# Optimization experiments

Hardware: AMD Instinct MI355X
Metric: run time of the kernel (lower is better)

## Reference

```python
import jax, jax.numpy as jnp
import numpy as np

B = 64  # batch_size (number of graphs)


def _leaky(v):
    return jax.nn.leaky_relu(v, 0.01)


def _gine(x, src, dst, edge_attr, ew, eb, w1, b1, w2, b2):
    # GINEConv (eps=0): out = nn(x + sum_{j->i} relu(x_j + lin(edge_attr)))
    n = x.shape[0]
    msg = jax.nn.relu(x[src] + edge_attr @ ew + eb)      # [E, C]
    agg = jax.ops.segment_sum(msg, dst, num_segments=n)  # [N, C]
    h = x + agg
    h = _leaky(h @ w1 + b1)
    h = _leaky(h @ w2 + b2)
    return h


def setup_inputs() -> dict:
    key = jax.random.key(0)
    ks = jax.random.split(key, 32)
    N, E, NF, EF, H, A = 65536, 1048576, 32, 16, 128, 10
    s = 0.05
    inp = {
        'x': jax.random.normal(ks[0], (N, NF), jnp.float32),
        'edge_index': jax.random.randint(ks[1], (2, E), 0, N, jnp.int64)
        if jax.config.jax_enable_x64 else jax.random.randint(ks[1], (2, E), 0, N, jnp.int32),
        'edge_attr': jax.random.normal(ks[2], (E, EF), jnp.float32),
        'e1_w': jax.random.normal(ks[3], (EF, NF)) * s, 'e1_b': jnp.zeros((NF,)),
        'c1_w1': jax.random.normal(ks[4], (NF, H)) * s, 'c1_b1': jnp.zeros((H,)),
        'c1_w2': jax.random.normal(ks[5], (H, H)) * s, 'c1_b2': jnp.zeros((H,)),
        'e2_w': jax.random.normal(ks[6], (EF, H)) * s, 'e2_b': jnp.zeros((H,)),
        'c2_w1': jax.random.normal(ks[7], (H, H)) * s, 'c2_b1': jnp.zeros((H,)),
        'c2_w2': jax.random.normal(ks[8], (H, H)) * s, 'c2_b2': jnp.zeros((H,)),
        'a_w1': jax.random.normal(ks[9], (H, H)) * s, 'a_b1': jnp.zeros((H,)),
        'a_w2': jax.random.normal(ks[10], (H, A)) * s, 'a_b2': jnp.zeros((A,)),
        'n_w1': jax.random.normal(ks[11], (H, H)) * s, 'n_b1': jnp.zeros((H,)),
        'n_w2': jax.random.normal(ks[12], (H, H)) * s, 'n_b2': jnp.zeros((H,)),
        'n_w3': jax.random.normal(ks[13], (H, 1)) * s, 'n_b3': jnp.zeros((1,)),
    }
    return inp


def reference(x, edge_index, edge_attr,
              e1_w, e1_b, c1_w1, c1_b1, c1_w2, c1_b2,
              e2_w, e2_b, c2_w1, c2_b1, c2_w2, c2_b2,
              a_w1, a_b1, a_w2, a_b2,
              n_w1, n_b1, n_w2, n_b2, n_w3, n_b3):
    src, dst = edge_index[0], edge_index[1]
    h = _gine(x, src, dst, edge_attr, e1_w, e1_b, c1_w1, c1_b1, c1_w2, c1_b2)
    h = jax.nn.relu(h)  # dropout is identity in eval mode
    h = _gine(h, src, dst, edge_attr, e2_w, e2_b, c2_w1, c2_b1, c2_w2, c2_b2)
    H = h.shape[-1]
    hb = h.reshape(B, -1, H)            # [B, Nper, H]
    pooled = hb.mean(axis=1)            # [B, H]
    a = _leaky(_leaky(pooled @ a_w1 + a_b1) @ a_w2 + a_b2)
    action_prob = jax.nn.softmax(a, axis=1)
    # reinterpret flat node order as [Nper, B, H], as in the torch reshape
    xr = h.reshape(-1, B, H)
    nh = _leaky(xr @ n_w1 + n_b1)
    nh = _leaky(nh @ n_w2 + n_b2)
    node_scores = jax.nn.sigmoid(nh @ n_w3 + n_b3)[..., 0].T  # [B, Nper]
    return action_prob, node_scores
```

## Files before the change

### kernel.cpp

```cpp
#include <hip/hip_runtime.h>
#include <math.h>

#define NNODES 65536
#define NEDGES 1048576
#define NF 32
#define EF 16
#define HD 128
#define NACT 10
#define NB 64
#define NPER 1024

typedef unsigned short u16;
typedef float  vf2  __attribute__((ext_vector_type(2)));
typedef float  vf4  __attribute__((ext_vector_type(4)));
typedef __bf16 vbf8 __attribute__((ext_vector_type(8)));
#define BC8(v) __builtin_bit_cast(vbf8, v)
#define WB() __builtin_amdgcn_wave_barrier()

__device__ __forceinline__ float leakyf(float v) { return v > 0.0f ? v : 0.01f * v; }
__device__ __forceinline__ vf2 fma2(vf2 a, vf2 b, vf2 c) { return __builtin_elementwise_fma(a, b, c); }
__device__ __forceinline__ vf2 max2(vf2 a, vf2 b) { return __builtin_elementwise_max(a, b); }
__device__ __forceinline__ vf2 splat2(float s) { vf2 r = {s, s}; return r; }

__device__ __forceinline__ u16 f2bf(float x) {
    unsigned u = __float_as_uint(x);
    return (u16)((u + 0x7FFFu + ((u >> 16) & 1u)) >> 16);
}
__device__ __forceinline__ float bf2f(u16 h) { return __uint_as_float(((unsigned)h) << 16); }

__device__ __forceinline__ void cvt4(const float4 s, uint2& hi, uint2& lo) {
    const u16 h0 = f2bf(s.x), h1 = f2bf(s.y), h2 = f2bf(s.z), h3 = f2bf(s.w);
    hi = make_uint2((unsigned)h0 | ((unsigned)h1 << 16), (unsigned)h2 | ((unsigned)h3 << 16));
    const u16 l0 = f2bf(s.x - bf2f(h0)), l1 = f2bf(s.y - bf2f(h1));
    const u16 l2 = f2bf(s.z - bf2f(h2)), l3 = f2bf(s.w - bf2f(h3));
    lo = make_uint2((unsigned)l0 | ((unsigned)l1 << 16), (unsigned)l2 | ((unsigned)l3 << 16));
}
__device__ __forceinline__ uint2 cvt4hi(const float4 s) {
    const u16 h0 = f2bf(s.x), h1 = f2bf(s.y), h2 = f2bf(s.z), h3 = f2bf(s.w);
    return make_uint2((unsigned)h0 | ((unsigned)h1 << 16), (unsigned)h2 | ((unsigned)h3 << 16));
}

__global__ __launch_bounds__(256) void hist_kernel(const int* __restrict__ ei, int* __restrict__ cnt)
{
    const int i = blockIdx.x * 256 + threadIdx.x;
    if (i < NEDGES) atomicAdd(&cnt[ei[NEDGES + i]], 1);
}

__global__ __launch_bounds__(1024) void scan_kernel(const int* __restrict__ cnt, int* __restrict__ rs)
{
    __shared__ int s[1024];
    const int t = threadIdx.x;
    int loc[64];
    int tot = 0;
    const int4* c4 = (const int4*)(cnt + t * 64);
    #pragma unroll
    for (int j = 0; j < 16; ++j) {
        const int4 v = c4[j];
        loc[4*j+0] = v.x; loc[4*j+1] = v.y; loc[4*j+2] = v.z; loc[4*j+3] = v.w;
        tot += v.x + v.y + v.z + v.w;
    }
    s[t] = tot;
    __syncthreads();
    for (int off = 1; off < 1024; off <<= 1) {
        const int v = (t >= off) ? s[t - off] : 0;
        __syncthreads();
        s[t] += v;
        __syncthreads();
    }
    int run = s[t] - tot;
    #pragma unroll
    for (int j = 0; j < 64; ++j) { rs[t * 64 + j] = run; run += loc[j]; }
    if (t == 0) rs[NNODES] = NEDGES;
}

__global__ __launch_bounds__(256) void scatter_kernel(
    const int* __restrict__ ei, const int* __restrict__ rs, int* __restrict__ fill,
    int* __restrict__ ssrc, int* __restrict__ seidx)
{
    const int i = blockIdx.x * 256 + threadIdx.x;
    if (i < NEDGES) {
        const int d = ei[NEDGES + i];
        const int pos = rs[d] + atomicAdd(&fill[d], 1);
        ssrc[pos]  = ei[i];
        seidx[pos] = i;
    }
}

__global__ __launch_bounds__(256) void permute_kernel(
    const int* __restrict__ seidx, const float* __restrict__ ea, float* __restrict__ sea)
{
    const int t = blockIdx.x * 256 + threadIdx.x;
    const int e = t >> 2, part = t & 3;
    const int idx = seidx[e];
    ((float4*)sea)[(size_t)e * 4 + part] = ((const float4*)ea)[(size_t)idx * 4 + part];
}

__global__ __launch_bounds__(256) void pack_all_kernel(
    const float* __restrict__ w0, const float* __restrict__ w1, const float* __restrict__ w2,
    const float* __restrict__ w3, const float* __restrict__ w4, const float* __restrict__ w5,
    u16* __restrict__ pw)
{
    const int bid = blockIdx.x;
    const float* W; int KB, seg, sbase;
    if (bid < 16) { W = w0; KB = 1; seg = 0; sbase = 0; }
    else {
        const int i = (bid - 16) >> 6;
        seg = i + 1; sbase = 16 + i * 64; KB = 4;
        W = (i == 0) ? w1 : (i == 1) ? w2 : (i == 2) ? w3 : (i == 3) ? w4 : w5;
    }
    const int t = (bid - sbase) * 256 + threadIdx.x;
    const int j = t & 7, lane = (t >> 3) & 63, rest = t >> 9;
    const int kb = rest % KB, fb = rest / KB;
    if (fb >= 8) return;
    const int k = kb * 32 + (lane >> 4) * 8 + j;
    const int f = fb * 16 + (lane & 15);
    const float val = W[k * HD + f];
    const u16 h = f2bf(val);
    u16* dst = pw + seg * 32768;
    dst[t] = h;
    dst[16384 + t] = f2bf(val - bf2f(h));
}

__global__ __launch_bounds__(256) void e1_agg_kernel(
    const float* __restrict__ x, const int* __restrict__ rs,
    const int* __restrict__ ssrc, const float* __restrict__ sea,
    const float* __restrict__ w, const float* __restrict__ b, float* __restrict__ agg)
{
    const int tid  = threadIdx.x;
    const int lane = tid & 63;
    const int p    = lane & 15;
    const int q    = lane >> 4;
    const int node = blockIdx.x * 4 + (tid >> 6);
    vf2 wr[EF];
    #pragma unroll
    for (int k = 0; k < EF; ++k) wr[k] = *(const vf2*)&w[k * NF + p * 2];
    const vf2 bias = *(const vf2*)&b[p * 2];
    const int beg = rs[node], end = rs[node + 1];
    vf2 acc = {0.0f, 0.0f};
    for (int e = beg + q; e < end; e += 4) {
        const int sA = ssrc[e];
        const float4* pA = (const float4*)sea + (size_t)e * 4;
        const float4 A0 = pA[0], A1 = pA[1], A2 = pA[2], A3 = pA[3];
        const vf2 xv = *(const vf2*)((const char*)x + (((unsigned)sA << 7) + (unsigned)p * 8));
        vf2 m = bias;
        m = fma2(splat2(A0.x), wr[0],  m); m = fma2(splat2(A0.y), wr[1],  m);
        m = fma2(splat2(A0.z), wr[2],  m); m = fma2(splat2(A0.w), wr[3],  m);
        m = fma2(splat2(A1.x), wr[4],  m); m = fma2(splat2(A1.y), wr[5],  m);
        m = fma2(splat2(A1.z), wr[6],  m); m = fma2(splat2(A1.w), wr[7],  m);
        m = fma2(splat2(A2.x), wr[8],  m); m = fma2(splat2(A2.y), wr[9],  m);
        m = fma2(splat2(A2.z), wr[10], m); m = fma2(splat2(A2.w), wr[11], m);
        m = fma2(splat2(A3.x), wr[12], m); m = fma2(splat2(A3.y), wr[13], m);
        m = fma2(splat2(A3.z), wr[14], m); m = fma2(splat2(A3.w), wr[15], m);
        acc += max2(xv + m, splat2(0.0f));
    }
    acc[0] += __shfl_xor(acc[0], 16, 64); acc[1] += __shfl_xor(acc[1], 16, 64);
    acc[0] += __shfl_xor(acc[0], 32, 64); acc[1] += __shfl_xor(acc[1], 32, 64);
    if (lane < 16) *(vf2*)&agg[(size_t)node * NF + p * 2] = acc;
}

__global__ __launch_bounds__(256) void e2_agg_kernel(
    const float* __restrict__ h, const int* __restrict__ rs,
    const int* __restrict__ ssrc, const float* __restrict__ sea,
    const float* __restrict__ w, const float* __restrict__ b, float* __restrict__ agg)
{
    const int tid  = threadIdx.x;
    const int lane = tid & 63;
    const unsigned foff = (unsigned)lane * 8;
    const int node = blockIdx.x * 4 + (tid >> 6);
    vf2 wr[EF];
    #pragma unroll
    for (int k = 0; k < EF; ++k) wr[k] = *(const vf2*)&w[k * HD + lane * 2];
    const vf2 bias = *(const vf2*)&b[lane * 2];
    const int beg = __builtin_amdgcn_readfirstlane(rs[node]);
    const int end = __builtin_amdgcn_readfirstlane(rs[node + 1]);
    vf2 acc = {0.0f, 0.0f};
    int e = beg;
    for (; e + 2 <= end; e += 2) {
        const int sA = ssrc[e];
        const int sB = ssrc[e + 1];
        const vf2 hA = *(const vf2*)((const char*)h + (((unsigned)sA << 9) + foff));
        const vf2 hB = *(const vf2*)((const char*)h + (((unsigned)sB << 9) + foff));
        const float* aA = &sea[(size_t)e * EF];
        const float* aB = aA + EF;
        vf2 mA = bias, mB = bias;
        #pragma unroll
        for (int k = 0; k < EF; ++k) {
            mA = fma2(splat2(aA[k]), wr[k], mA);
            mB = fma2(splat2(aB[k]), wr[k], mB);
        }
        acc += max2(hA + mA, splat2(0.0f));
        acc += max2(hB + mB, splat2(0.0f));
    }
    if (e < end) {
        const int sA = ssrc[e];
        const vf2 hA = *(const vf2*)((const char*)h + (((unsigned)sA << 9) + foff));
        const float* aA = &sea[(size_t)e * EF];
        vf2 mA = bias;
        #pragma unroll
        for (int k = 0; k < EF; ++k) mA = fma2(splat2(aA[k]), wr[k], mA);
        acc += max2(hA + mA, splat2(0.0f));
    }
    *(vf2*)&agg[(size_t)node * HD + lane * 2] = acc;
}

#define ROW128 272
#define ROW32  80

__device__ __forceinline__ void mfma_layer128_in(
    const unsigned char* __restrict__ aH, const unsigned char* __restrict__ aL,
    const u16* __restrict__ wH, const u16* __restrict__ wL,
    const float* __restrict__ bias, int lane, vf4* __restrict__ acc)
{
    const int quad = lane >> 4, fm = lane & 15;
    int4 Bh[4], Bl[4];
    #pragma unroll
    for (int kb = 0; kb < 4; ++kb) {
        Bh[kb] = *(const int4*)(aH + fm * ROW128 + kb * 64 + quad * 16);
        Bl[kb] = *(const int4*)(aL + fm * ROW128 + kb * 64 + quad * 16);
    }
    #pragma unroll
    for (int fb = 0; fb < 8; ++fb) {
        const float4 bv = *(const float4*)&bias[fb * 16 + quad * 4];
        vf4 a = {bv.x, bv.y, bv.z, bv.w};
        #pragma unroll
        for (int kb = 0; kb < 4; ++kb) {
            const int4 wh = *(const int4*)(wH + ((fb * 4 + kb) * 64 + lane) * 8);
            const int4 wl = *(const int4*)(wL + ((fb * 4 + kb) * 64 + lane) * 8);
            a = __builtin_amdgcn_mfma_f32_16x16x32_bf16(BC8(wh), BC8(Bl[kb]), a, 0, 0, 0);
            a = __builtin_amdgcn_mfma_f32_16x16x32_bf16(BC8(wl), BC8(Bh[kb]), a, 0, 0, 0);
            a = __builtin_amdgcn_mfma_f32_16x16x32_bf16(BC8(wh), BC8(Bh[kb]), a, 0, 0, 0);
        }
        acc[fb] = a;
    }
}

__device__ __forceinline__ void mfma_layer128_act(
    const unsigned char* __restrict__ aH,
    const u16* __restrict__ wH, const u16* __restrict__ wL,
    const float* __restrict__ bias, int lane, vf4* __restrict__ acc)
{
    const int quad = lane >> 4, fm = lane & 15;
    int4 Bh[4];
    #pragma unroll
    for (int kb = 0; kb < 4; ++kb)
        Bh[kb] = *(const int4*)(aH + fm * ROW128 + kb * 64 + quad * 16);
    #pragma unroll
    for (int fb = 0; fb < 8; ++fb) {
        const float4 bv = *(const float4*)&bias[fb * 16 + quad * 4];
        vf4 a = {bv.x, bv.y, bv.z, bv.w};
        #pragma unroll
        for (int kb = 0; kb < 4; ++kb) {
            const int4 wh = *(const int4*)(wH + ((fb * 4 + kb) * 64 + lane) * 8);
            const int4 wl = *(const int4*)(wL + ((fb * 4 + kb) * 64 + lane) * 8);
            a = __builtin_amdgcn_mfma_f32_16x16x32_bf16(BC8(wl), BC8(Bh[kb]), a, 0, 0, 0);
            a = __builtin_amdgcn_mfma_f32_16x16x32_bf16(BC8(wh), BC8(Bh[kb]), a, 0, 0, 0);
        }
        acc[fb] = a;
    }
}

__device__ __forceinline__ void mfma_layer32_in(
    const unsigned char* __restrict__ aH, const unsigned char* __restrict__ aL,
    const u16* __restrict__ wH, const u16* __restrict__ wL,
    const float* __restrict__ bias, int lane, vf4* __restrict__ acc)
{
    const int quad = lane >> 4, fm = lane & 15;
    const int4 Bh = *(const int4*)(aH + fm * ROW32 + quad * 16);
    const int4 Bl = *(const int4*)(aL + fm * ROW32 + quad * 16);
    #pragma unroll
    for (int fb = 0; fb < 8; ++fb) {
        const float4 bv = *(const float4*)&bias[fb * 16 + quad * 4];
        vf4 a = {bv.x, bv.y, bv.z, bv.w};
        const int4 wh = *(const int4*)(wH + (fb * 64 + lane) * 8);
        const int4 wl = *(const int4*)(wL + (fb * 64 + lane) * 8);
        a = __builtin_amdgcn_mfma_f32_16x16x32_bf16(BC8(wh), BC8(Bl), a, 0, 0, 0);
        a = __builtin_amdgcn_mfma_f32_16x16x32_bf16(BC8(wl), BC8(Bh), a, 0, 0, 0);
        a = __builtin_amdgcn_mfma_f32_16x16x32_bf16(BC8(wh), BC8(Bh), a, 0, 0, 0);
        acc[fb] = a;
    }
}

__device__ __forceinline__ void store_act_hi(
    unsigned char* __restrict__ aH, int lane, vf4* __restrict__ acc)
{
    const int quad = lane >> 4, fm = lane & 15;
    #pragma unroll
    for (int fb = 0; fb < 8; ++fb) {
        const float4 s = {leakyf(acc[fb][0]), leakyf(acc[fb][1]), leakyf(acc[fb][2]), leakyf(acc[fb][3])};
        acc[fb][0] = s.x; acc[fb][1] = s.y; acc[fb][2] = s.z; acc[fb][3] = s.w;
        *(uint2*)(aH + fm * ROW128 + fb * 32 + quad * 8) = cvt4hi(s);
    }
}

__global__ __launch_bounds__(256) void n1_kernel(
    const float* __restrict__ x, const float* __restrict__ agg,
    const u16* __restrict__ w1h, const u16* __restrict__ w1l, const float* __restrict__ b1,
    const u16* __restrict__ w2h, const u16* __restrict__ w2l, const float* __restrict__ b2,
    float* __restrict__ hout)
{
    __shared__ __align__(16) unsigned char smem[4][2560 + 16 * ROW128];
    const int tid = threadIdx.x, lane = tid & 63, wid = tid >> 6;
    const int quad = lane >> 4, fm = lane & 15;
    const int tile = blockIdx.x * 4 + wid;
    unsigned char* inH = smem[wid];
    unsigned char* inL = inH + 16 * ROW32;
    unsigned char* aH  = inH + 2560;
    const size_t base = (size_t)tile * 16 * NF;
    #pragma unroll
    for (int i = 0; i < 2; ++i) {
        const int flat = i * 64 + lane;
        const int node = flat >> 3, kq = flat & 7;
        const float4 xv = *(const float4*)&x[base + node * NF + kq * 4];
        const float4 av = *(const float4*)&agg[base + node * NF + kq * 4];
        const float4 s = {xv.x + av.x, xv.y + av.y, xv.z + av.z, xv.w + av.w};
        uint2 phi, plo;
        cvt4(s, phi, plo);
        *(uint2*)(inH + node * ROW32 + kq * 8) = phi;
        *(uint2*)(inL + node * ROW32 + kq * 8) = plo;
    }
    WB();
    vf4 acc[8];
    mfma_layer32_in(inH, inL, w1h, w1l, b1, lane, acc);
    WB();
    store_act_hi(aH, lane, acc);
    WB();
    mfma_layer128_act(aH, w2h, w2l, b2, lane, acc);
    const size_t ob = (size_t)tile * 16 * HD;
    #pragma unroll
    for (int fb = 0; fb < 8; ++fb) {
        const float4 o = {fmaxf(acc[fb][0], 0.0f), fmaxf(acc[fb][1], 0.0f),
                          fmaxf(acc[fb][2], 0.0f), fmaxf(acc[fb][3], 0.0f)};
        *(float4*)&hout[ob + fm * HD + fb * 16 + quad * 4] = o;
    }
}

__global__ __launch_bounds__(256) void n2_kernel(
    const float* __restrict__ h, const float* __restrict__ agg,
    const u16* __restrict__ w1h, const u16* __restrict__ w1l, const float* __restrict__ b1,
    const u16* __restrict__ w2h, const u16* __restrict__ w2l, const float* __restrict__ b2,
    const u16* __restrict__ m1h, const u16* __restrict__ m1l, const float* __restrict__ nb1,
    const u16* __restrict__ m2h, const u16* __restrict__ m2l, const float* __restrict__ nb2,
    const float* __restrict__ nw3, const float* __restrict__ nb3,
    float* __restrict__ pooled, float* __restrict__ scores)
{
    __shared__ __align__(16) unsigned char smem[4][2 * 16 * ROW128];
    const int tid = threadIdx.x, lane = tid & 63, wid = tid >> 6;
    const int quad = lane >> 4, fm = lane & 15;
    const int tile = blockIdx.x * 4 + wid;
    unsigned char* aH = smem[wid];
    unsigned char* aL = aH + 16 * ROW128;
    const size_t base = (size_t)tile * 16 * HD;
    #pragma unroll
    for (int i = 0; i < 8; ++i) {
        const int flat = i * 64 + lane;
        const int node = flat >> 5, kq = flat & 31;
        const float4 hv = *(const float4*)&h[base + node * HD + kq * 4];
        const float4 av = *(const float4*)&agg[base + node * HD + kq * 4];
        const float4 s = {hv.x + av.x, hv.y + av.y, hv.z + av.z, hv.w + av.w};
        uint2 phi, plo;
        cvt4(s, phi, plo);
        *(uint2*)(aH + node * ROW128 + kq * 8) = phi;
        *(uint2*)(aL + node * ROW128 + kq * 8) = plo;
    }
    WB();
    vf4 acc[8];
    mfma_layer128_in(aH, aL, w1h, w1l, b1, lane, acc);
    WB();
    store_act_hi(aH, lane, acc);
    WB();
    mfma_layer128_act(aH, w2h, w2l, b2, lane, acc);
    WB();
    store_act_hi(aH, lane, acc);
    {
        const int g = tile >> 6;
        #pragma unroll
        for (int fb = 0; fb < 8; ++fb) {
            vf4 t = acc[fb];
            #pragma unroll
            for (int off = 1; off < 16; off <<= 1) {
                t[0] += __shfl_xor(t[0], off, 64);
                t[1] += __shfl_xor(t[1], off, 64);
                t[2] += __shfl_xor(t[2], off, 64);
                t[3] += __shfl_xor(t[3], off, 64);
            }
            #pragma unroll
            for (int r = 0; r < 4; ++r) {
                const int item = fb * 4 + r;
                if (fm == (item >> 1))
                    atomicAdd(&pooled[g * HD + fb * 16 + quad * 4 + r], t[r]);
            }
        }
    }
    WB();
    mfma_layer128_act(aH, m1h, m1l, nb1, lane, acc);
    WB();
    store_act_hi(aH, lane, acc);
    WB();
    mfma_layer128_act(aH, m2h, m2l, nb2, lane, acc);
    float v = 0.0f;
    #pragma unroll
    for (int fb = 0; fb < 8; ++fb) {
        const float4 w3v = *(const float4*)&nw3[fb * 16 + quad * 4];
        v += leakyf(acc[fb][0]) * w3v.x + leakyf(acc[fb][1]) * w3v.y
           + leakyf(acc[fb][2]) * w3v.z + leakyf(acc[fb][3]) * w3v.w;
    }
    v += __shfl_xor(v, 16, 64);
    v += __shfl_xor(v, 32, 64);
    if (lane < 16) {
        const int node = tile * 16 + fm;
        const float s = v + nb3[0];
        scores[(node & 63) * NPER + (node >> 6)] = 1.0f / (1.0f + expf(-s));
    }
}

__global__ __launch_bounds__(128) void act_kernel(
    const float* __restrict__ pooled,
    const float* __restrict__ w1, const float* __restrict__ b1,
    const float* __restrict__ w2, const float* __restrict__ b2,
    float* __restrict__ out)
{
    __shared__ __align__(16) float p[HD];
    __shared__ float a1[HD];
    __shared__ float z[NACT];
    __shared__ float red2[2];
    const int g = blockIdx.x;
    const int tid = threadIdx.x;
    p[tid] = pooled[g * HD + tid] * (1.0f / NPER);
    __syncthreads();
    float acc = b1[tid];
    for (int k = 0; k < HD; ++k) acc = fmaf(p[k], w1[k * HD + tid], acc);
    a1[tid] = leakyf(acc);
    __syncthreads();
    if (tid < NACT) {
        float a2 = b2[tid];
        for (int k = 0; k < HD; ++k) a2 = fmaf(a1[k], w2[k * NACT + tid], a2);
        z[tid] = leakyf(a2);
    }
    __syncthreads();
    if (tid == 0) {
        float m = z[0];
        for (int i = 1; i < NACT; ++i) m = fmaxf(m, z[i]);
        red2[0] = m;
    }
    __syncthreads();
    if (tid < NACT) z[tid] = expf(z[tid] - red2[0]);
    __syncthreads();
    if (tid == 0) {
        float s = 0.0f;
        for (int i = 0; i < NACT; ++i) s += z[i];
        red2[1] = s;
    }
    __syncthreads();
    if (tid < NACT) out[g * NACT + tid] = z[tid] / red2[1];
}

extern "C" void kernel_launch(void* const* d_in, const int* in_sizes, int n_in,
                              void* d_out, int out_size, void* d_ws, size_t ws_size,
                              hipStream_t stream)
{
    const float* x    = (const float*)d_in[0];
    const int*   ei   = (const int*)d_in[1];
    const float* ea   = (const float*)d_in[2];
    const float* e1w  = (const float*)d_in[3];
    const float* e1b  = (const float*)d_in[4];
    const float* c1w1 = (const float*)d_in[5];
    const float* c1b1 = (const float*)d_in[6];
    const float* c1w2 = (const float*)d_in[7];
    const float* c1b2 = (const float*)d_in[8];
    const float* e2w  = (const float*)d_in[9];
    const float* e2b  = (const float*)d_in[10];
    const float* c2w1 = (const float*)d_in[11];
    const float* c2b1 = (const float*)d_in[12];
    const float* c2w2 = (const float*)d_in[13];
    const float* c2b2 = (const float*)d_in[14];
    const float* aw1  = (const float*)d_in[15];
    const float* ab1  = (const float*)d_in[16];
    const float* aw2  = (const float*)d_in[17];
    const float* ab2  = (const float*)d_in[18];
    const float* nw1  = (const float*)d_in[19];
    const float* nb1  = (const float*)d_in[20];
    const float* nw2  = (const float*)d_in[21];
    const float* nb2  = (const float*)d_in[22];
    const float* nw3  = (const float*)d_in[23];
    const float* nb3  = (const float*)d_in[24];

    float* out = (float*)d_out;
    char*  ws  = (char*)d_ws;
    const size_t MB = 1024 * 1024;
    float* h      = (float*)(ws);
    float* agg2   = (float*)(ws + 32  * MB);
    int*   seidx  = (int*)  (ws + 32  * MB);
    float* sea    = (float*)(ws + 64  * MB);
    float* agg1   = (float*)(ws + 128 * MB);
    float* pooled = (float*)(ws + 136 * MB);
    u16*   pw     = (u16*)  (ws + 136 * MB + 64 * 1024);
    int*   cnt    = (int*)  (ws + 137 * MB);
    int*   fill   = (int*)  (ws + 137 * MB + 256 * 1024);
    int*   rs     = (int*)  (ws + 139 * MB);
    int*   ssrc   = (int*)  (ws + 140 * MB);

    u16* p_c1w1 = pw;
    u16* p_c1w2 = pw + 1 * 32768;
    u16* p_c2w1 = pw + 2 * 32768;
    u16* p_c2w2 = pw + 3 * 32768;
    u16* p_nw1  = pw + 4 * 32768;
    u16* p_nw2  = pw + 5 * 32768;

    hipMemsetAsync(cnt,    0, 2 * NNODES * sizeof(int), stream);
    hipMemsetAsync(pooled, 0, (size_t)NB * HD * sizeof(float), stream);

    pack_all_kernel<<<336, 256, 0, stream>>>(c1w1, c1w2, c2w1, c2w2, nw1, nw2, pw);

    hist_kernel<<<NEDGES / 256, 256, 0, stream>>>(ei, cnt);
    scan_kernel<<<1, 1024, 0, stream>>>(cnt, rs);
    scatter_kernel<<<NEDGES / 256, 256, 0, stream>>>(ei, rs, fill, ssrc, seidx);
    permute_kernel<<<NEDGES / 64, 256, 0, stream>>>(seidx, ea, sea);

    e1_agg_kernel<<<NNODES / 4, 256, 0, stream>>>(x, rs, ssrc, sea, e1w, e1b, agg1);
    n1_kernel<<<NNODES / 64, 256, 0, stream>>>(x, agg1,
                                               p_c1w1, p_c1w1 + 16384, c1b1,
                                               p_c1w2, p_c1w2 + 16384, c1b2, h);
    e2_agg_kernel<<<NNODES / 4, 256, 0, stream>>>(h, rs, ssrc, sea, e2w, e2b, agg2);
    n2_kernel<<<NNODES / 64, 256, 0, stream>>>(h, agg2,
                                               p_c2w1, p_c2w1 + 16384, c2b1,
                                               p_c2w2, p_c2w2 + 16384, c2b2,
                                               p_nw1,  p_nw1  + 16384, nb1,
                                               p_nw2,  p_nw2  + 16384, nb2,
                                               nw3, nb3, pooled, out + NB * NACT);
    act_kernel<<<NB, 128, 0, stream>>>(pooled, aw1, ab1, aw2, ab2, out);
}
```

Measured before the change: 576.9 us.

## Coalesce edge-attr loads in e1 aggregation and broadcast via ds_swizzle

Rewrites the e1 aggregation loop so that each wave loads edge attributes as coalesced scalar floats, one per lane, instead of four redundant float4 loads per lane. Each attribute is then broadcast within its 16-lane group using ds_swizzle for the FMA chain. Source indices are loaded once per 64-edge window and distributed with shuffles, and the row bounds are made wave-uniform with readfirstlane. This aims to cut redundant global memory traffic, at the cost of extra cross-lane operations and more complex tail handling.

```diff
diff --git a/kernel.cpp b/kernel.cpp
--- a/kernel.cpp
+++ b/kernel.cpp
@@ -38,6 +38,14 @@
 __device__ __forceinline__ uint2 cvt4hi(const float4 s) {
     const u16 h0 = f2bf(s.x), h1 = f2bf(s.y), h2 = f2bf(s.z), h3 = f2bf(s.w);
     return make_uint2((unsigned)h0 | ((unsigned)h1 << 16), (unsigned)h2 | ((unsigned)h3 << 16));
+}
+
+template<int K>
+__device__ __forceinline__ void bcast16_fma(const float av, const vf2* __restrict__ wr, vf2& m) {
+    const float a = __uint_as_float((unsigned)__builtin_amdgcn_ds_swizzle(
+        (int)__float_as_uint(av), (K << 5) | 0x10));
+    m = fma2(splat2(a), wr[K], m);
+    if constexpr (K + 1 < EF) bcast16_fma<K + 1>(av, wr, m);
 }
 
 __global__ __launch_bounds__(256) void hist_kernel(const int* __restrict__ ei, int* __restrict__ cnt)
@@ -135,23 +143,47 @@
     #pragma unroll
     for (int k = 0; k < EF; ++k) wr[k] = *(const vf2*)&w[k * NF + p * 2];
     const vf2 bias = *(const vf2*)&b[p * 2];
-    const int beg = rs[node], end = rs[node + 1];
+    const int beg = __builtin_amdgcn_readfirstlane(rs[node]);
+    const int end = __builtin_amdgcn_readfirstlane(rs[node + 1]);
     vf2 acc = {0.0f, 0.0f};
-    for (int e = beg + q; e < end; e += 4) {
-        const int sA = ssrc[e];
-        const float4* pA = (const float4*)sea + (size_t)e * 4;
-        const float4 A0 = pA[0], A1 = pA[1], A2 = pA[2], A3 = pA[3];
-        const vf2 xv = *(const vf2*)((const char*)x + (((unsigned)sA << 7) + (unsigned)p * 8));
-        vf2 m = bias;
-        m = fma2(splat2(A0.x), wr[0],  m); m = fma2(splat2(A0.y), wr[1],  m);
-        m = fma2(splat2(A0.z), wr[2],  m); m = fma2(splat2(A0.w), wr[3],  m);
-        m = fma2(splat2(A1.x), wr[4],  m); m = fma2(splat2(A1.y), wr[5],  m);
-        m = fma2(splat2(A1.z), wr[6],  m); m = fma2(splat2(A1.w), wr[7],  m);
-        m = fma2(splat2(A2.x), wr[8],  m); m = fma2(splat2(A2.y), wr[9],  m);
-        m = fma2(splat2(A2.z), wr[10], m); m = fma2(splat2(A2.w), wr[11], m);
-        m = fma2(splat2(A3.x), wr[12], m); m = fma2(splat2(A3.y), wr[13], m);
-        m = fma2(splat2(A3.z), wr[14], m); m = fma2(splat2(A3.w), wr[15], m);
-        acc += max2(xv + m, splat2(0.0f));
+    for (int wnd = beg; wnd < end; wnd += 64) {
+        const int nw = min(end - wnd, 64);
+        const int srcL = (lane < nw) ? ssrc[wnd + lane] : 0;
+        const float* sbase = sea + (size_t)wnd * EF;
+        int blk = 0;
+        for (; blk + 16 <= nw; blk += 16) {
+            float av[4];
+            #pragma unroll
+            for (int u = 0; u < 4; ++u)
+                av[u] = sbase[blk * EF + u * 64 + lane];
+            vf2 xv[4];
+            #pragma unroll
+            for (int u = 0; u < 4; ++u) {
+                const int sA = __shfl(srcL, blk + u * 4 + q, 64);
+                xv[u] = *(const vf2*)((const char*)x + (((unsigned)sA << 7) + (unsigned)p * 8));
+            }
+            #pragma unroll
+            for (int u = 0; u < 4; ++u) {
+                vf2 m = bias;
+                bcast16_fma<0>(av[u], wr, m);
+                acc += max2(xv[u] + m, splat2(0.0f));
+            }
+        }
+        const int nrem = nw - blk;
+        if (nrem > 0) {
+            #pragma unroll
+            for (int u = 0; u < 4; ++u) {
+                if (u * 4 >= nrem) break;
+                const int myidx = u * 4 + q;
+                const bool valid = myidx < nrem;
+                const float av = valid ? sbase[blk * EF + u * 64 + lane] : 0.0f;
+                const int sA = __shfl(srcL, min(blk + myidx, nw - 1), 64);
+                const vf2 xv = *(const vf2*)((const char*)x + (((unsigned)sA << 7) + (unsigned)p * 8));
+                vf2 m = bias;
+                bcast16_fma<0>(av, wr, m);
+                if (valid) acc += max2(xv + m, splat2(0.0f));
+            }
+        }
     }
     acc[0] += __shfl_xor(acc[0], 16, 64); acc[1] += __shfl_xor(acc[1], 16, 64);
     acc[0] += __shfl_xor(acc[0], 32, 64); acc[1] += __shfl_xor(acc[1], 32, 64);
```

After: 557.5 us. 1.03x faster.
